# Kernel optimization log

Measured on AMD Instinct MI355X. Metric: run time of the kernel, lower is better.

## Reference

```python
import jax, jax.numpy as jnp
import numpy as np

# dims: batch, parity, l-dims of in1/in2, output l-dim, channels
B, P, L1, L2, N, F = 8192, 2, 9, 9, 25, 128

MASK_EVEN = jnp.array([[1.0], [0.0]], dtype=jnp.float32)  # [2,1]
MASK_ODD = jnp.array([[0.0], [1.0]], dtype=jnp.float32)   # [2,1]


def setup_inputs() -> dict:
    key = jax.random.key(0)
    k1, k2, k3 = jax.random.split(key, 3)
    x1 = jax.random.normal(k1, (B, P, L1, F), dtype=jnp.float32)
    x2 = jax.random.normal(k2, (B, P, L2, F), dtype=jnp.float32)
    # Clebsch-Gordan tensor is an nn.Parameter in the module; random init is
    # equivalent for correctness testing of the contraction math.
    cg = jax.random.normal(k3, (L1, L2, N), dtype=jnp.float32)
    return {"x1": x1, "x2": x2, "cg": cg}


def reference(x1, x2, cg):
    # pseudotensor path of TensorProduct.forward with channel_dim='f'
    def couple(m1, m2):
        a = jnp.einsum('bplf,pa->balf', x1, m1)  # parity mask projection, a=1
        b = jnp.einsum('bplf,pa->balf', x2, m2)
        # triple contraction against CG tensor: [B,1,N,F]
        return jnp.einsum('balf,bamf,lmn->banf', a, b, cg)

    # NOTE: original code calls _couple_slices('even','odd') for BOTH eee and
    # eoo — reproduced faithfully.
    eee = couple(MASK_EVEN, MASK_ODD)
    ooe = couple(MASK_ODD, MASK_EVEN)
    eoo = couple(MASK_EVEN, MASK_ODD)
    oeo = couple(MASK_ODD, MASK_ODD)
    # stack along axis=-3 -> [B, 1, 2, N, F]
    return jnp.stack((eee + ooe, eoo + oeo), axis=-3)
```

## Files before the change

### kernel.cpp

```cpp
#include <hip/hip_runtime.h>


#define B_DIM 8192
#define F_DIM 128
#define L_DIM 9
#define N_DIM 25

typedef __attribute__((ext_vector_type(2))) float v2f;

__global__ __launch_bounds__(256) void tp_kernel(
    const float* __restrict__ x1,
    const float* __restrict__ x2,
    const float* __restrict__ cg,
    float* __restrict__ out)
{
    const int g = blockIdx.x * 256 + threadIdx.x;
    const int b = g >> 7;
    const int f = g & 127;

    const float* x1b = x1 + (size_t)b * 2 * L_DIM * F_DIM + f;
    const float* x2b = x2 + (size_t)b * 2 * L_DIM * F_DIM + f;

    v2f x2p[L_DIM];
#pragma unroll
    for (int m = 0; m < L_DIM; ++m) {
        v2f v;
        v.x = __builtin_nontemporal_load(&x2b[m * F_DIM]);
        v.y = __builtin_nontemporal_load(&x2b[(L_DIM + m) * F_DIM]);
        x2p[m] = v;
    }

    v2f acc[N_DIM];
#pragma unroll
    for (int n = 0; n < N_DIM; ++n) { acc[n] = (v2f)(0.0f); }

#pragma unroll 1
    for (int l = 0; l < L_DIM; ++l) {
        const float x1e = __builtin_nontemporal_load(&x1b[l * F_DIM]);
        const float x1o = __builtin_nontemporal_load(&x1b[(L_DIM + l) * F_DIM]);
        v2f x1o2; x1o2.x = x1o; x1o2.y = x1o;
        const float* cp_l = cg + l * (L_DIM * N_DIM);
#pragma unroll
        for (int m = 0; m < L_DIM; ++m) {
            const float t = x1e * x2p[m].y;
            v2f tt; tt.x = t; tt.y = t;
            const v2f s = __builtin_elementwise_fma(x1o2, x2p[m], tt);
#pragma unroll
            for (int n = 0; n < N_DIM; ++n) {
                const float c = cp_l[m * N_DIM + n];
                v2f cc; cc.x = c; cc.y = c;
                acc[n] = __builtin_elementwise_fma(cc, s, acc[n]);
            }
        }
    }

    float* ob = out + (size_t)b * 2 * N_DIM * F_DIM + f;
#pragma unroll
    for (int n = 0; n < N_DIM; ++n) {
        __builtin_nontemporal_store(acc[n].x, &ob[n * F_DIM]);
        __builtin_nontemporal_store(acc[n].y, &ob[(N_DIM + n) * F_DIM]);
    }
}

extern "C" void kernel_launch(void* const* d_in, const int* in_sizes, int n_in,
                              void* d_out, int out_size, void* d_ws, size_t ws_size,
                              hipStream_t stream) {
    (void)in_sizes; (void)n_in; (void)out_size; (void)d_ws; (void)ws_size;
    const float* x1 = (const float*)d_in[0];
    const float* x2 = (const float*)d_in[1];
    const float* cg = (const float*)d_in[2];
    float* out = (float*)d_out;

    const int threads = 256;
    const int blocks  = (B_DIM * F_DIM) / threads;
    tp_kernel<<<blocks, threads, 0, stream>>>(x1, x2, cg, out);
}
```

Baseline: 344.8 us.

## Process two channels per thread and stage CG tensor in padded shared memory

Each thread now computes two adjacent channels, halving the grid and reusing each CG coefficient across four FMAs. The CG tensor is copied into LDS with rows padded to 28 so coefficients can be read as float4 vectors instead of scalar global loads. The changes add register pressure (100 accumulator floats plus inputs), which may reduce occupancy, and a per-block shared-memory fill and barrier.

```diff
diff --git a/kernel.cpp b/kernel.cpp
--- a/kernel.cpp
+++ b/kernel.cpp
@@ -5,8 +5,16 @@
 #define F_DIM 128
 #define L_DIM 9
 #define N_DIM 25
+#define NPAD 28
 
 typedef __attribute__((ext_vector_type(2))) float v2f;
+
+__device__ __forceinline__ v2f ntload2(const float* p) {
+    v2f v;
+    v.x = __builtin_nontemporal_load(p);
+    v.y = __builtin_nontemporal_load(p + 1);
+    return v;
+}
 
 __global__ __launch_bounds__(256) void tp_kernel(
     const float* __restrict__ x1,
@@ -14,51 +22,69 @@
     const float* __restrict__ cg,
     float* __restrict__ out)
 {
+    __shared__ float cgs[L_DIM * L_DIM * NPAD];
+
+    for (int i = threadIdx.x; i < L_DIM * L_DIM * N_DIM; i += 256) {
+        const int r = i / N_DIM;
+        const int c = i - r * N_DIM;
+        cgs[r * NPAD + c] = cg[i];
+    }
+    __syncthreads();
+
     const int g = blockIdx.x * 256 + threadIdx.x;
-    const int b = g >> 7;
-    const int f = g & 127;
+    const int b = g >> 6;
+    const int f = (g & 63) << 1;
 
     const float* x1b = x1 + (size_t)b * 2 * L_DIM * F_DIM + f;
     const float* x2b = x2 + (size_t)b * 2 * L_DIM * F_DIM + f;
 
-    v2f x2p[L_DIM];
+    v2f x2e2[L_DIM], x2o2[L_DIM];
 #pragma unroll
     for (int m = 0; m < L_DIM; ++m) {
-        v2f v;
-        v.x = __builtin_nontemporal_load(&x2b[m * F_DIM]);
-        v.y = __builtin_nontemporal_load(&x2b[(L_DIM + m) * F_DIM]);
-        x2p[m] = v;
+        x2e2[m] = ntload2(x2b + m * F_DIM);
+        x2o2[m] = ntload2(x2b + (L_DIM + m) * F_DIM);
     }
 
-    v2f acc[N_DIM];
+    v2f acc0[N_DIM], acc1[N_DIM];
 #pragma unroll
-    for (int n = 0; n < N_DIM; ++n) { acc[n] = (v2f)(0.0f); }
+    for (int n = 0; n < N_DIM; ++n) { acc0[n] = (v2f)(0.0f); acc1[n] = (v2f)(0.0f); }
 
 #pragma unroll 1
     for (int l = 0; l < L_DIM; ++l) {
-        const float x1e = __builtin_nontemporal_load(&x1b[l * F_DIM]);
-        const float x1o = __builtin_nontemporal_load(&x1b[(L_DIM + l) * F_DIM]);
-        v2f x1o2; x1o2.x = x1o; x1o2.y = x1o;
-        const float* cp_l = cg + l * (L_DIM * N_DIM);
+        const v2f x1e2 = ntload2(x1b + l * F_DIM);
+        const v2f x1o2 = ntload2(x1b + (L_DIM + l) * F_DIM);
+        const float* cl = &cgs[l * (L_DIM * NPAD)];
 #pragma unroll
         for (int m = 0; m < L_DIM; ++m) {
-            const float t = x1e * x2p[m].y;
-            v2f tt; tt.x = t; tt.y = t;
-            const v2f s = __builtin_elementwise_fma(x1o2, x2p[m], tt);
+            const v2f t  = x1e2 * x2o2[m];
+            const v2f s0 = __builtin_elementwise_fma(x1o2, x2e2[m], t);
+            const v2f s1 = __builtin_elementwise_fma(x1o2, x2o2[m], t);
+            const float* cm = cl + m * NPAD;
 #pragma unroll
-            for (int n = 0; n < N_DIM; ++n) {
-                const float c = cp_l[m * N_DIM + n];
-                v2f cc; cc.x = c; cc.y = c;
-                acc[n] = __builtin_elementwise_fma(cc, s, acc[n]);
+            for (int q = 0; q < 6; ++q) {
+                const float4 c4 = *reinterpret_cast<const float4*>(cm + q * 4);
+                acc0[q*4+0] = __builtin_elementwise_fma((v2f)(c4.x), s0, acc0[q*4+0]);
+                acc1[q*4+0] = __builtin_elementwise_fma((v2f)(c4.x), s1, acc1[q*4+0]);
+                acc0[q*4+1] = __builtin_elementwise_fma((v2f)(c4.y), s0, acc0[q*4+1]);
+                acc1[q*4+1] = __builtin_elementwise_fma((v2f)(c4.y), s1, acc1[q*4+1]);
+                acc0[q*4+2] = __builtin_elementwise_fma((v2f)(c4.z), s0, acc0[q*4+2]);
+                acc1[q*4+2] = __builtin_elementwise_fma((v2f)(c4.z), s1, acc1[q*4+2]);
+                acc0[q*4+3] = __builtin_elementwise_fma((v2f)(c4.w), s0, acc0[q*4+3]);
+                acc1[q*4+3] = __builtin_elementwise_fma((v2f)(c4.w), s1, acc1[q*4+3]);
             }
+            const float c24 = cm[24];
+            acc0[24] = __builtin_elementwise_fma((v2f)(c24), s0, acc0[24]);
+            acc1[24] = __builtin_elementwise_fma((v2f)(c24), s1, acc1[24]);
         }
     }
 
     float* ob = out + (size_t)b * 2 * N_DIM * F_DIM + f;
 #pragma unroll
     for (int n = 0; n < N_DIM; ++n) {
-        __builtin_nontemporal_store(acc[n].x, &ob[n * F_DIM]);
-        __builtin_nontemporal_store(acc[n].y, &ob[(N_DIM + n) * F_DIM]);
+        __builtin_nontemporal_store(acc0[n].x, ob + n * F_DIM);
+        __builtin_nontemporal_store(acc0[n].y, ob + n * F_DIM + 1);
+        __builtin_nontemporal_store(acc1[n].x, ob + (N_DIM + n) * F_DIM);
+        __builtin_nontemporal_store(acc1[n].y, ob + (N_DIM + n) * F_DIM + 1);
     }
 }
 
@@ -72,6 +98,6 @@
     float* out = (float*)d_out;
 
     const int threads = 256;
-    const int blocks  = (B_DIM * F_DIM) / threads;
+    const int blocks  = (B_DIM * (F_DIM / 2)) / threads;
     tp_kernel<<<blocks, threads, 0, stream>>>(x1, x2, cg, out);
 }
```

Measured after the change: 363.4 us. +5.4%, slower.

## Pad CG rows to pairs and vectorize FMA over output pairs

Applied to the files above, without the earlier changes.

A small prep kernel copies the CG tensor into a global buffer padded to 26 columns, so each pair of n values can be fetched as one aligned 8-byte scalar load. The main loop now packs pairs of CG coefficients (along n) into a v2f and uses separate accumulators for the even and odd outputs. The per-lane s vector is replaced by broadcast scalars, which cuts CG scalar loads roughly in half while keeping the packed FMA count about the same. Nontemporal loads on the inputs are also dropped. The cost is an extra kernel launch and one padded dummy column per row.

```diff
diff --git a/kernel.cpp b/kernel.cpp
--- a/kernel.cpp
+++ b/kernel.cpp
@@ -5,13 +5,24 @@
 #define F_DIM 128
 #define L_DIM 9
 #define N_DIM 25
+#define NROW 26
+#define NPAIR 13
 
 typedef __attribute__((ext_vector_type(2))) float v2f;
+
+__device__ __align__(16) float g_cgp[L_DIM * L_DIM * NROW];
+
+__global__ __launch_bounds__(256) void cg_prep(const float* __restrict__ cg) {
+    for (int i = threadIdx.x; i < L_DIM * L_DIM * NROW; i += 256) {
+        const int row = i / NROW;
+        const int c   = i - row * NROW;
+        g_cgp[i] = (c < N_DIM) ? cg[row * N_DIM + c] : 0.0f;
+    }
+}
 
 __global__ __launch_bounds__(256) void tp_kernel(
     const float* __restrict__ x1,
     const float* __restrict__ x2,
-    const float* __restrict__ cg,
     float* __restrict__ out)
 {
     const int g = blockIdx.x * 256 + threadIdx.x;
@@ -21,44 +32,52 @@
     const float* x1b = x1 + (size_t)b * 2 * L_DIM * F_DIM + f;
     const float* x2b = x2 + (size_t)b * 2 * L_DIM * F_DIM + f;
 
-    v2f x2p[L_DIM];
+    float x2e[L_DIM], x2o[L_DIM];
 #pragma unroll
     for (int m = 0; m < L_DIM; ++m) {
-        v2f v;
-        v.x = __builtin_nontemporal_load(&x2b[m * F_DIM]);
-        v.y = __builtin_nontemporal_load(&x2b[(L_DIM + m) * F_DIM]);
-        x2p[m] = v;
+        x2e[m] = x2b[m * F_DIM];
+        x2o[m] = x2b[(L_DIM + m) * F_DIM];
     }
 
-    v2f acc[N_DIM];
+    v2f acc0[NPAIR], acc1[NPAIR];
 #pragma unroll
-    for (int n = 0; n < N_DIM; ++n) { acc[n] = (v2f)(0.0f); }
+    for (int q = 0; q < NPAIR; ++q) { acc0[q] = (v2f)(0.0f); acc1[q] = (v2f)(0.0f); }
+
+    const float* __restrict__ cgp = g_cgp;
 
 #pragma unroll 1
     for (int l = 0; l < L_DIM; ++l) {
-        const float x1e = __builtin_nontemporal_load(&x1b[l * F_DIM]);
-        const float x1o = __builtin_nontemporal_load(&x1b[(L_DIM + l) * F_DIM]);
-        v2f x1o2; x1o2.x = x1o; x1o2.y = x1o;
-        const float* cp_l = cg + l * (L_DIM * N_DIM);
+        const float x1e = x1b[l * F_DIM];
+        const float x1o = x1b[(L_DIM + l) * F_DIM];
+        const float* cl = cgp + l * (L_DIM * NROW);
 #pragma unroll
         for (int m = 0; m < L_DIM; ++m) {
-            const float t = x1e * x2p[m].y;
-            v2f tt; tt.x = t; tt.y = t;
-            const v2f s = __builtin_elementwise_fma(x1o2, x2p[m], tt);
+            const float t  = x1e * x2o[m];
+            const float s0 = fmaf(x1o, x2e[m], t);
+            const float s1 = fmaf(x1o, x2o[m], t);
+            v2f s0v; s0v.x = s0; s0v.y = s0;
+            v2f s1v; s1v.x = s1; s1v.y = s1;
+            const float* cm = cl + m * NROW;
 #pragma unroll
-            for (int n = 0; n < N_DIM; ++n) {
-                const float c = cp_l[m * N_DIM + n];
-                v2f cc; cc.x = c; cc.y = c;
-                acc[n] = __builtin_elementwise_fma(cc, s, acc[n]);
+            for (int q = 0; q < NPAIR; ++q) {
+                v2f c2;
+                c2.x = cm[q * 2];
+                c2.y = cm[q * 2 + 1];
+                acc0[q] = __builtin_elementwise_fma(c2, s0v, acc0[q]);
+                acc1[q] = __builtin_elementwise_fma(c2, s1v, acc1[q]);
             }
         }
     }
 
     float* ob = out + (size_t)b * 2 * N_DIM * F_DIM + f;
 #pragma unroll
-    for (int n = 0; n < N_DIM; ++n) {
-        __builtin_nontemporal_store(acc[n].x, &ob[n * F_DIM]);
-        __builtin_nontemporal_store(acc[n].y, &ob[(N_DIM + n) * F_DIM]);
+    for (int q = 0; q < NPAIR; ++q) {
+        __builtin_nontemporal_store(acc0[q].x, ob + (2 * q) * F_DIM);
+        __builtin_nontemporal_store(acc1[q].x, ob + (N_DIM + 2 * q) * F_DIM);
+        if (q < NPAIR - 1) {
+            __builtin_nontemporal_store(acc0[q].y, ob + (2 * q + 1) * F_DIM);
+            __builtin_nontemporal_store(acc1[q].y, ob + (N_DIM + 2 * q + 1) * F_DIM);
+        }
     }
 }
 
@@ -71,7 +90,9 @@
     const float* cg = (const float*)d_in[2];
     float* out = (float*)d_out;
 
+    cg_prep<<<1, 256, 0, stream>>>(cg);
+
     const int threads = 256;
     const int blocks  = (B_DIM * F_DIM) / threads;
-    tp_kernel<<<blocks, threads, 0, stream>>>(x1, x2, cg, out);
+    tp_kernel<<<blocks, threads, 0, stream>>>(x1, x2, out);
 }
```

New measurement: 338.7 us. About the same (-1.8%).

## Pack CG pairs to fp16 and accumulate with packed dot2 instructions

Applied to the files above, without the earlier changes.

Adds a prep kernel that converts the CG tensor to fp16 and packs adjacent (l,m) pairs into 32-bit words in a device global, read through the constant address space. The main kernel fully unrolls over lm pairs, converts the products s to packed half, and accumulates with v_dot2 (fp16 x fp16 -> fp32), halving the FMA count. It also loads all inputs up front and sets a launch-bounds occupancy hint. The cost is lower precision in the CG coefficients and the products, plus a small extra kernel launch.

```diff
diff --git a/kernel.cpp b/kernel.cpp
--- a/kernel.cpp
+++ b/kernel.cpp
@@ -1,17 +1,40 @@
 #include <hip/hip_runtime.h>
+#include <stdint.h>
 
 
 #define B_DIM 8192
 #define F_DIM 128
 #define L_DIM 9
 #define N_DIM 25
+#define LM_DIM 81
+#define KPAIR 41
+#define CROW 28
 
-typedef __attribute__((ext_vector_type(2))) float v2f;
+typedef const __attribute__((address_space(4))) uint32_t* cu32p4;
+using h2_t = decltype(__builtin_amdgcn_cvt_pkrtz(0.0f, 0.0f));
 
-__global__ __launch_bounds__(256) void tp_kernel(
+__device__ __align__(16) uint32_t g_cgp2[KPAIR * CROW];
+
+__global__ __launch_bounds__(256) void cg_prep(const float* __restrict__ cg) {
+    for (int i = threadIdx.x; i < KPAIR * CROW; i += 256) {
+        const int a = i / CROW;
+        const int n = i - a * CROW;
+        uint32_t packed = 0;
+        if (n < N_DIM) {
+            const int lm0 = 2 * a, lm1 = 2 * a + 1;
+            _Float16 h0 = (_Float16)cg[lm0 * N_DIM + n];
+            _Float16 h1 = (lm1 < LM_DIM) ? (_Float16)cg[lm1 * N_DIM + n]
+                                         : (_Float16)0.0f;
+            packed = (uint32_t)__builtin_bit_cast(uint16_t, h0) |
+                     ((uint32_t)__builtin_bit_cast(uint16_t, h1) << 16);
+        }
+        g_cgp2[i] = packed;
+    }
+}
+
+__global__ __launch_bounds__(256, 4) void tp_kernel(
     const float* __restrict__ x1,
     const float* __restrict__ x2,
-    const float* __restrict__ cg,
     float* __restrict__ out)
 {
     const int g = blockIdx.x * 256 + threadIdx.x;
@@ -21,44 +44,58 @@
     const float* x1b = x1 + (size_t)b * 2 * L_DIM * F_DIM + f;
     const float* x2b = x2 + (size_t)b * 2 * L_DIM * F_DIM + f;
 
-    v2f x2p[L_DIM];
+    float x1e[L_DIM], x1o[L_DIM], x2e[L_DIM], x2o[L_DIM];
 #pragma unroll
-    for (int m = 0; m < L_DIM; ++m) {
-        v2f v;
-        v.x = __builtin_nontemporal_load(&x2b[m * F_DIM]);
-        v.y = __builtin_nontemporal_load(&x2b[(L_DIM + m) * F_DIM]);
-        x2p[m] = v;
+    for (int l = 0; l < L_DIM; ++l) {
+        x1e[l] = x1b[l * F_DIM];
+        x1o[l] = x1b[(L_DIM + l) * F_DIM];
+        x2e[l] = x2b[l * F_DIM];
+        x2o[l] = x2b[(L_DIM + l) * F_DIM];
     }
 
-    v2f acc[N_DIM];
+    float acc0[N_DIM], acc1[N_DIM];
 #pragma unroll
-    for (int n = 0; n < N_DIM; ++n) { acc[n] = (v2f)(0.0f); }
+    for (int n = 0; n < N_DIM; ++n) { acc0[n] = 0.0f; acc1[n] = 0.0f; }
 
-#pragma unroll 1
-    for (int l = 0; l < L_DIM; ++l) {
-        const float x1e = __builtin_nontemporal_load(&x1b[l * F_DIM]);
-        const float x1o = __builtin_nontemporal_load(&x1b[(L_DIM + l) * F_DIM]);
-        v2f x1o2; x1o2.x = x1o; x1o2.y = x1o;
-        const float* cp_l = cg + l * (L_DIM * N_DIM);
+    const cu32p4 cgp = (cu32p4)(uintptr_t)&g_cgp2[0];
+
 #pragma unroll
-        for (int m = 0; m < L_DIM; ++m) {
-            const float t = x1e * x2p[m].y;
-            v2f tt; tt.x = t; tt.y = t;
-            const v2f s = __builtin_elementwise_fma(x1o2, x2p[m], tt);
+    for (int a = 0; a < KPAIR; ++a) {
+        const int lm0 = 2 * a, lm1 = 2 * a + 1;
+        const int l0 = lm0 / L_DIM, m0 = lm0 % L_DIM;
+        const float t0  = x1e[l0] * x2o[m0];
+        const float s0a = fmaf(x1o[l0], x2e[m0], t0);
+        const float s1a = fmaf(x1o[l0], x2o[m0], t0);
+        float s0b = 0.0f, s1b = 0.0f;
+        if (lm1 < LM_DIM) {
+            const int l1 = lm1 / L_DIM, m1 = lm1 % L_DIM;
+            const float t1 = x1e[l1] * x2o[m1];
+            s0b = fmaf(x1o[l1], x2e[m1], t1);
+            s1b = fmaf(x1o[l1], x2o[m1], t1);
+        }
+        const h2_t s0p = __builtin_amdgcn_cvt_pkrtz(s0a, s0b);
+        const h2_t s1p = __builtin_amdgcn_cvt_pkrtz(s1a, s1b);
 #pragma unroll
-            for (int n = 0; n < N_DIM; ++n) {
-                const float c = cp_l[m * N_DIM + n];
-                v2f cc; cc.x = c; cc.y = c;
-                acc[n] = __builtin_elementwise_fma(cc, s, acc[n]);
-            }
+        for (int n = 0; n < N_DIM; ++n) {
+            const uint32_t cv = cgp[a * CROW + n];
+            const h2_t ch = __builtin_bit_cast(h2_t, cv);
+#if __has_builtin(__builtin_amdgcn_fdot2)
+            acc0[n] = __builtin_amdgcn_fdot2(ch, s0p, acc0[n], false);
+            acc1[n] = __builtin_amdgcn_fdot2(ch, s1p, acc1[n], false);
+#else
+            acc0[n] = fmaf((float)ch[0], (float)s0p[0],
+                      fmaf((float)ch[1], (float)s0p[1], acc0[n]));
+            acc1[n] = fmaf((float)ch[0], (float)s1p[0],
+                      fmaf((float)ch[1], (float)s1p[1], acc1[n]));
+#endif
         }
     }
 
     float* ob = out + (size_t)b * 2 * N_DIM * F_DIM + f;
 #pragma unroll
     for (int n = 0; n < N_DIM; ++n) {
-        __builtin_nontemporal_store(acc[n].x, &ob[n * F_DIM]);
-        __builtin_nontemporal_store(acc[n].y, &ob[(N_DIM + n) * F_DIM]);
+        __builtin_nontemporal_store(acc0[n], ob + n * F_DIM);
+        __builtin_nontemporal_store(acc1[n], ob + (N_DIM + n) * F_DIM);
     }
 }
 
@@ -71,7 +108,9 @@
     const float* cg = (const float*)d_in[2];
     float* out = (float*)d_out;
 
+    cg_prep<<<1, 256, 0, stream>>>(cg);
+
     const int threads = 256;
     const int blocks  = (B_DIM * F_DIM) / threads;
-    tp_kernel<<<blocks, threads, 0, stream>>>(x1, x2, cg, out);
+    tp_kernel<<<blocks, threads, 0, stream>>>(x1, x2, out);
 }
```

New measurement: 348.5 us. About the same (+1.1%).
